# Performance work log

Hardware: AMD Instinct MI355X
Metric: run time of the kernel (lower is better)

Reference implementation:

```python
import jax, jax.numpy as jnp
import numpy as np

TEMP = 1.0
NUM_HEADS = 4


def tropical_linear(x, W, b, temperature=TEMP):
    # x: (..., in), W: (out, in), b: (out,)
    # y_i = T * logsumexp_j((W_ij + x_j)/T) + b_i  (soft tropical max-plus)
    z = W + x[..., None, :]                      # (..., out, in) broadcast tensor
    y = temperature * jax.nn.logsumexp(z / temperature, axis=-1)
    return y + b


def setup_inputs() -> dict:
    key = jax.random.key(0)
    ks = jax.random.split(key, 5)
    B, S, E = 32, 64, 256  # seq_len == head_dim (= E / num_heads) required by original code
    x = jax.random.normal(ks[0], (B, S, E), dtype=jnp.float32)
    mk = lambda k: 0.1 * jax.random.normal(k, (E, E), dtype=jnp.float32)
    zb = jnp.zeros((E,), dtype=jnp.float32)
    return {
        "x": x,
        "Wq": mk(ks[1]), "bq": zb,
        "Wk": mk(ks[2]), "bk": zb,
        "Wv": mk(ks[3]), "bv": zb,
        "Wo": mk(ks[4]), "bo": zb,
    }


def reference(x, Wq, bq, Wk, bk, Wv, bv, Wo, bo):
    B, S, E = x.shape
    H = NUM_HEADS
    D = E // H  # == S by construction (required by original matmul)

    q = tropical_linear(x, Wq, bq)  # (B,S,E)
    k = tropical_linear(x, Wk, bk)
    v = tropical_linear(x, Wv, bv)

    # (B,S,E) -> (B,H,S,D)
    split = lambda t: t.reshape(B, S, H, D).transpose(0, 2, 1, 3)
    q, k, v = split(q), split(k), split(v)

    # Original: (q.unsqueeze(-1) + k.unsqueeze(-2).transpose(-1,-2)).sum(-1)
    # Both operands are (B,H,S,D,1) -> scores == q + k elementwise, shape (B,H,S,D).
    scores = q + k
    attn = jax.nn.softmax(scores / TEMP, axis=-1)  # (B,H,S,D)

    # matmul (B,H,S,D) @ (B,H,S,D) valid since D == S
    out = jnp.einsum('bhsd,bhde->bhse', attn, v)   # (B,H,S,D)
    out = out.transpose(0, 2, 1, 3).reshape(B, S, E)
    return tropical_linear(out, Wo, bo)
```

## Files before the change

kernel.cpp:

```cpp
#include <hip/hip_runtime.h>

constexpr int ED = 256;
constexpr int SD = 64;
constexpr int BD = 32;
constexpr int NROWS = BD * SD;

typedef _Float16 half8 __attribute__((ext_vector_type(8)));
typedef float floatx4 __attribute__((ext_vector_type(4)));

__device__ inline unsigned short f2h(float f) {
  union { _Float16 h; unsigned short u; } c;
  c.h = (_Float16)f;
  return c.u;
}

__global__ __launch_bounds__(256) void expT_swz_kernel(
    const float* __restrict__ Wq, const float* __restrict__ Wk,
    const float* __restrict__ Wv, const float* __restrict__ Wo,
    unsigned short* __restrict__ EqS, unsigned short* __restrict__ EkS,
    unsigned short* __restrict__ EvS, unsigned short* __restrict__ EoS)
{
  int z = blockIdx.y;
  const float* W = (z == 0) ? Wq : (z == 1) ? Wk : (z == 2) ? Wv : Wo;
  unsigned short* out = (z == 0) ? EqS : (z == 1) ? EkS : (z == 2) ? EvS : EoS;
  int t = threadIdx.x;
  int n = blockIdx.x * 8 + (t >> 5), kl = t & 31;
#pragma unroll
  for (int kk = 0; kk < 8; ++kk)
    out[(kk * 256 + n) * 32 + kl] = f2h(__expf(W[n * ED + 32 * kk + kl]));
}

__global__ __launch_bounds__(256, 2) void qkv_mfma_kernel(
    const float* __restrict__ x,
    const unsigned short* __restrict__ EqS, const unsigned short* __restrict__ EkS,
    const unsigned short* __restrict__ EvS,
    const float* __restrict__ bq, const float* __restrict__ bk,
    const float* __restrict__ bv,
    unsigned short* __restrict__ AS, unsigned short* __restrict__ VS)
{
  int t = threadIdx.x;
  int w = t >> 6, lane = t & 63;
  int mt = blockIdx.x >> 2, h = blockIdx.x & 3;
  int row0 = mt * 16;

  __shared__ unsigned short aswz[8 * 512];
  __shared__ float fbuf[3][16][65];
  __shared__ float Mrow[16];

  float4 xv[4];
#pragma unroll
  for (int i = 0; i < 4; ++i)
    xv[i] = *(const float4*)&x[(size_t)(row0 + 4 * w + i) * ED + lane * 4];

  int bb = ((h * 64 + w * 16 + (lane & 15)) << 2) + (lane >> 4);
  const half8* BQ = (const half8*)EqS;
  const half8* BK = (const half8*)EkS;
  const half8* BV = (const half8*)EvS;
  half8 bqf[8], bkf[8], bvf[8];
#pragma unroll
  for (int kk = 0; kk < 8; ++kk) {
    bqf[kk] = BQ[kk * 1024 + bb];
    bkf[kk] = BK[kk * 1024 + bb];
    bvf[kk] = BV[kk * 1024 + bb];
  }

#pragma unroll
  for (int i = 0; i < 4; ++i) {
    int r = 4 * w + i;
    float m = fmaxf(fmaxf(xv[i].x, xv[i].y), fmaxf(xv[i].z, xv[i].w));
#pragma unroll
    for (int off = 32; off > 0; off >>= 1) m = fmaxf(m, __shfl_xor(m, off));
    ushort4 pk;
    pk.x = f2h(__expf(xv[i].x - m));
    pk.y = f2h(__expf(xv[i].y - m));
    pk.z = f2h(__expf(xv[i].z - m));
    pk.w = f2h(__expf(xv[i].w - m));
    int k0 = lane * 4;
    int idx = (k0 >> 5) * 512 + ((k0 >> 3) & 3) * 128 + r * 8 + (k0 & 7);
    *(ushort4*)&aswz[idx] = pk;
    if (lane == 0) Mrow[r] = m;
  }
  __syncthreads();

  half8 afrag[8];
#pragma unroll
  for (int kk = 0; kk < 8; ++kk)
    afrag[kk] = *(const half8*)&aswz[kk * 512 + lane * 8];

  floatx4 accq = {0.f, 0.f, 0.f, 0.f};
  floatx4 acck = {0.f, 0.f, 0.f, 0.f};
  floatx4 accv = {0.f, 0.f, 0.f, 0.f};
#pragma unroll
  for (int kk = 0; kk < 8; ++kk) {
    accq = __builtin_amdgcn_mfma_f32_16x16x32_f16(afrag[kk], bqf[kk], accq, 0, 0, 0);
    acck = __builtin_amdgcn_mfma_f32_16x16x32_f16(afrag[kk], bkf[kk], acck, 0, 0, 0);
    accv = __builtin_amdgcn_mfma_f32_16x16x32_f16(afrag[kk], bvf[kk], accv, 0, 0, 0);
  }

  {
    int c = w * 16 + (lane & 15);
    int rb = (lane >> 4) * 4;
#pragma unroll
    for (int reg = 0; reg < 4; ++reg) {
      fbuf[0][rb + reg][c] = accq[reg];
      fbuf[1][rb + reg][c] = acck[reg];
      fbuf[2][rb + reg][c] = accv[reg];
    }
  }
  __syncthreads();

  int cg = h * 64 + lane;
  float bqv = bq[cg], bkv = bk[cg], bvv = bv[cg];
  int b = row0 >> 6;
  int mt16 = (row0 >> 4) & 3;
  size_t asBase = (size_t)(((b * 4 + mt16) * 4) + h) * 1024
                + (lane >> 5) * 512 + ((lane >> 3) & 3) * 128 + (lane & 7);
#pragma unroll
  for (int i = 0; i < 4; ++i) {
    int r = 4 * w + i;
    float Mr = Mrow[r];
    float qv = Mr + __logf(fbuf[0][r][lane]) + bqv;
    float kv = Mr + __logf(fbuf[1][r][lane]) + bkv;
    float vv = Mr + __logf(fbuf[2][r][lane]) + bvv;
    int d = mt16 * 16 + r;
    VS[(size_t)(b * 2 + (d >> 5)) * 8192 + cg * 32 + ((d >> 3) & 3) * 8 + (d & 7)]
        = f2h(vv);
    float s = qv + kv;
    float sm = s;
#pragma unroll
    for (int off = 32; off > 0; off >>= 1) sm = fmaxf(sm, __shfl_xor(sm, off));
    float ex = __expf(s - sm);
    float den = ex;
#pragma unroll
    for (int off = 32; off > 0; off >>= 1) den += __shfl_xor(den, off);
    AS[asBase + r * 8] = f2h(ex / den);
  }
}

__global__ __launch_bounds__(256, 2) void avo_mfma_kernel(
    const unsigned short* __restrict__ AS, const unsigned short* __restrict__ VS,
    const unsigned short* __restrict__ EoS, const float* __restrict__ bo,
    float* __restrict__ y)
{
  int t = threadIdx.x, w = t >> 6, lane = t & 63;
  int blk = blockIdx.x;
  int b = blk >> 3, mt = (blk >> 1) & 3, hf = blk & 1;
  int row0 = b * 64 + mt * 16;
  int q = lane >> 4, nl = lane & 15;

  __shared__ float obuf[16][260];
  __shared__ unsigned short easwz[8 * 512];
  __shared__ float Mrow[16];

  const half8* AS8 = (const half8*)(AS + (size_t)(((b * 4 + mt) * 4) + w) * 1024);
  const half8* VS8 = (const half8*)VS;
  half8 af0 = AS8[lane], af1 = AS8[64 + lane];
  floatx4 acc[4];
#pragma unroll
  for (int nt = 0; nt < 4; ++nt) acc[nt] = (floatx4){0.f, 0.f, 0.f, 0.f};
#pragma unroll
  for (int nt = 0; nt < 4; ++nt) {
    int n = w * 64 + nt * 16 + nl;
    half8 b0 = VS8[(size_t)(b * 2 + 0) * 1024 + n * 4 + q];
    half8 b1 = VS8[(size_t)(b * 2 + 1) * 1024 + n * 4 + q];
    acc[nt] = __builtin_amdgcn_mfma_f32_16x16x32_f16(af0, b0, acc[nt], 0, 0, 0);
    acc[nt] = __builtin_amdgcn_mfma_f32_16x16x32_f16(af1, b1, acc[nt], 0, 0, 0);
  }
  int rb = q * 4;
#pragma unroll
  for (int nt = 0; nt < 4; ++nt)
#pragma unroll
    for (int reg = 0; reg < 4; ++reg)
      obuf[rb + reg][w * 64 + nt * 16 + nl] = acc[nt][reg];
  __syncthreads();

#pragma unroll
  for (int i = 0; i < 4; ++i) {
    int r = 4 * w + i;
    float4 o4 = *(const float4*)&obuf[r][lane * 4];
    float m = fmaxf(fmaxf(o4.x, o4.y), fmaxf(o4.z, o4.w));
#pragma unroll
    for (int off = 32; off > 0; off >>= 1) m = fmaxf(m, __shfl_xor(m, off));
    ushort4 pk;
    pk.x = f2h(__expf(o4.x - m));
    pk.y = f2h(__expf(o4.y - m));
    pk.z = f2h(__expf(o4.z - m));
    pk.w = f2h(__expf(o4.w - m));
    int k0 = lane * 4;
    int idx = (k0 >> 5) * 512 + ((k0 >> 3) & 3) * 128 + r * 8 + (k0 & 7);
    *(ushort4*)&easwz[idx] = pk;
    if (lane == 0) Mrow[r] = m;
  }
  __syncthreads();

  half8 af2[8];
#pragma unroll
  for (int kk = 0; kk < 8; ++kk)
    af2[kk] = *(const half8*)&easwz[kk * 512 + lane * 8];
  const half8* BO = (const half8*)EoS;
  floatx4 acc2[2];
  acc2[0] = (floatx4){0.f, 0.f, 0.f, 0.f};
  acc2[1] = (floatx4){0.f, 0.f, 0.f, 0.f};
#pragma unroll
  for (int kk = 0; kk < 8; ++kk) {
#pragma unroll
    for (int nt = 0; nt < 2; ++nt) {
      int n = hf * 128 + w * 32 + nt * 16 + nl;
      acc2[nt] = __builtin_amdgcn_mfma_f32_16x16x32_f16(
          af2[kk], BO[kk * 1024 + n * 4 + q], acc2[nt], 0, 0, 0);
    }
  }
#pragma unroll
  for (int nt = 0; nt < 2; ++nt)
#pragma unroll
    for (int reg = 0; reg < 4; ++reg)
      obuf[rb + reg][hf * 128 + w * 32 + nt * 16 + nl] = acc2[nt][reg];
  __syncthreads();

  int c0 = hf * 128 + lane * 2;
  float2 bo2 = *(const float2*)&bo[c0];
#pragma unroll
  for (int i = 0; i < 4; ++i) {
    int r = 4 * w + i;
    float2 f2 = *(const float2*)&obuf[r][c0];
    float M = Mrow[r];
    float2 y2;
    y2.x = M + __logf(f2.x) + bo2.x;
    y2.y = M + __logf(f2.y) + bo2.y;
    *(float2*)&y[(size_t)(row0 + r) * ED + c0] = y2;
  }
}

extern "C" void kernel_launch(void* const* d_in, const int* in_sizes, int n_in,
                              void* d_out, int out_size, void* d_ws, size_t ws_size,
                              hipStream_t stream) {
  const float* x  = (const float*)d_in[0];
  const float* Wq = (const float*)d_in[1];
  const float* bq = (const float*)d_in[2];
  const float* Wk = (const float*)d_in[3];
  const float* bk = (const float*)d_in[4];
  const float* Wv = (const float*)d_in[5];
  const float* bv = (const float*)d_in[6];
  const float* Wo = (const float*)d_in[7];
  const float* bo = (const float*)d_in[8];
  float* y = (float*)d_out;

  char* ws = (char*)d_ws;
  unsigned short* EqS = (unsigned short*)(ws);
  unsigned short* EkS = (unsigned short*)(ws + 131072);
  unsigned short* EvS = (unsigned short*)(ws + 262144);
  unsigned short* EoS = (unsigned short*)(ws + 393216);
  unsigned short* AS  = (unsigned short*)(ws + 524288);
  unsigned short* VS  = (unsigned short*)(ws + 524288 + 1048576);

  expT_swz_kernel<<<dim3(32, 4), 256, 0, stream>>>(Wq, Wk, Wv, Wo,
                                                   EqS, EkS, EvS, EoS);
  qkv_mfma_kernel<<<512, 256, 0, stream>>>(x, EqS, EkS, EvS, bq, bk, bv,
                                           AS, VS);
  avo_mfma_kernel<<<256, 256, 0, stream>>>(AS, VS, EoS, bo, y);
}
```

Measured before the change: 86.20 us.

## Fuse QKV projection, attention and output projection into one per-batch kernel

Replaces the two MFMA kernels with a single kernel that handles one batch element per 512-thread block. Q/K/V, the softmax, attn·V and the output tropical projection all stay in shared memory, so the global round trip for the A and V intermediates and one launch are gone. The cost is a grid of only 32 blocks on a many-CU GPU, which leaves most compute units idle. Each wave also now streams all of the 128 output columns' weights through registers, raising register pressure.

```diff
diff --git a/kernel.cpp b/kernel.cpp
--- a/kernel.cpp
+++ b/kernel.cpp
@@ -1,9 +1,6 @@
 #include <hip/hip_runtime.h>
 
 constexpr int ED = 256;
-constexpr int SD = 64;
-constexpr int BD = 32;
-constexpr int NROWS = BD * SD;
 
 typedef _Float16 half8 __attribute__((ext_vector_type(8)));
 typedef float floatx4 __attribute__((ext_vector_type(4)));
@@ -30,43 +27,33 @@
     out[(kk * 256 + n) * 32 + kl] = f2h(__expf(W[n * ED + 32 * kk + kl]));
 }
 
-__global__ __launch_bounds__(256, 2) void qkv_mfma_kernel(
+__global__ __launch_bounds__(512, 1) void fused_attn_kernel(
     const float* __restrict__ x,
     const unsigned short* __restrict__ EqS, const unsigned short* __restrict__ EkS,
-    const unsigned short* __restrict__ EvS,
+    const unsigned short* __restrict__ EvS, const unsigned short* __restrict__ EoS,
     const float* __restrict__ bq, const float* __restrict__ bk,
-    const float* __restrict__ bv,
-    unsigned short* __restrict__ AS, unsigned short* __restrict__ VS)
+    const float* __restrict__ bv, const float* __restrict__ bo,
+    float* __restrict__ y)
 {
-  int t = threadIdx.x;
-  int w = t >> 6, lane = t & 63;
-  int mt = blockIdx.x >> 2, h = blockIdx.x & 3;
-  int row0 = mt * 16;
-
-  __shared__ unsigned short aswz[8 * 512];
-  __shared__ float fbuf[3][16][65];
-  __shared__ float Mrow[16];
-
-  float4 xv[4];
-#pragma unroll
-  for (int i = 0; i < 4; ++i)
-    xv[i] = *(const float4*)&x[(size_t)(row0 + 4 * w + i) * ED + lane * 4];
-
-  int bb = ((h * 64 + w * 16 + (lane & 15)) << 2) + (lane >> 4);
-  const half8* BQ = (const half8*)EqS;
-  const half8* BK = (const half8*)EkS;
-  const half8* BV = (const half8*)EvS;
-  half8 bqf[8], bkf[8], bvf[8];
-#pragma unroll
-  for (int kk = 0; kk < 8; ++kk) {
-    bqf[kk] = BQ[kk * 1024 + bb];
-    bkf[kk] = BK[kk * 1024 + bb];
-    bvf[kk] = BV[kk * 1024 + bb];
-  }
-
-#pragma unroll
-  for (int i = 0; i < 4; ++i) {
-    int r = 4 * w + i;
+  int t = threadIdx.x, w = t >> 6, lane = t & 63;
+  int b = blockIdx.x;
+  int q = lane >> 4, nl = lane & 15;
+  int rb = q * 4;
+
+  __shared__ unsigned short xoswz[4][4096];
+  __shared__ unsigned short aswz[4][4096];
+  __shared__ unsigned short vswz[4][4096];
+  __shared__ float Mrow[64];
+  __shared__ float pmax[8][64];
+  __shared__ float Omax[64];
+
+  float4 xv[8];
+#pragma unroll
+  for (int i = 0; i < 8; ++i)
+    xv[i] = *(const float4*)&x[(size_t)(b * 64 + w * 8 + i) * ED + lane * 4];
+#pragma unroll
+  for (int i = 0; i < 8; ++i) {
+    int r = w * 8 + i;
     float m = fmaxf(fmaxf(xv[i].x, xv[i].y), fmaxf(xv[i].z, xv[i].w));
 #pragma unroll
     for (int off = 32; off > 0; off >>= 1) m = fmaxf(m, __shfl_xor(m, off));
@@ -76,158 +63,180 @@
     pk.z = f2h(__expf(xv[i].z - m));
     pk.w = f2h(__expf(xv[i].w - m));
     int k0 = lane * 4;
-    int idx = (k0 >> 5) * 512 + ((k0 >> 3) & 3) * 128 + r * 8 + (k0 & 7);
-    *(ushort4*)&aswz[idx] = pk;
+    int idx = (k0 >> 5) * 512 + ((k0 >> 3) & 3) * 128 + (r & 15) * 8 + (k0 & 7);
+    *(ushort4*)&xoswz[r >> 4][idx] = pk;
     if (lane == 0) Mrow[r] = m;
   }
   __syncthreads();
 
-  half8 afrag[8];
-#pragma unroll
-  for (int kk = 0; kk < 8; ++kk)
-    afrag[kk] = *(const half8*)&aswz[kk * 512 + lane * 8];
-
-  floatx4 accq = {0.f, 0.f, 0.f, 0.f};
-  floatx4 acck = {0.f, 0.f, 0.f, 0.f};
-  floatx4 accv = {0.f, 0.f, 0.f, 0.f};
-#pragma unroll
-  for (int kk = 0; kk < 8; ++kk) {
-    accq = __builtin_amdgcn_mfma_f32_16x16x32_f16(afrag[kk], bqf[kk], accq, 0, 0, 0);
-    acck = __builtin_amdgcn_mfma_f32_16x16x32_f16(afrag[kk], bkf[kk], acck, 0, 0, 0);
-    accv = __builtin_amdgcn_mfma_f32_16x16x32_f16(afrag[kk], bvf[kk], accv, 0, 0, 0);
-  }
-
-  {
-    int c = w * 16 + (lane & 15);
-    int rb = (lane >> 4) * 4;
-#pragma unroll
-    for (int reg = 0; reg < 4; ++reg) {
-      fbuf[0][rb + reg][c] = accq[reg];
-      fbuf[1][rb + reg][c] = acck[reg];
-      fbuf[2][rb + reg][c] = accv[reg];
-    }
-  }
-  __syncthreads();
-
-  int cg = h * 64 + lane;
-  float bqv = bq[cg], bkv = bk[cg], bvv = bv[cg];
-  int b = row0 >> 6;
-  int mt16 = (row0 >> 4) & 3;
-  size_t asBase = (size_t)(((b * 4 + mt16) * 4) + h) * 1024
-                + (lane >> 5) * 512 + ((lane >> 3) & 3) * 128 + (lane & 7);
-#pragma unroll
-  for (int i = 0; i < 4; ++i) {
-    int r = 4 * w + i;
-    float Mr = Mrow[r];
-    float qv = Mr + __logf(fbuf[0][r][lane]) + bqv;
-    float kv = Mr + __logf(fbuf[1][r][lane]) + bkv;
-    float vv = Mr + __logf(fbuf[2][r][lane]) + bvv;
-    int d = mt16 * 16 + r;
-    VS[(size_t)(b * 2 + (d >> 5)) * 8192 + cg * 32 + ((d >> 3) & 3) * 8 + (d & 7)]
-        = f2h(vv);
-    float s = qv + kv;
-    float sm = s;
-#pragma unroll
-    for (int off = 32; off > 0; off >>= 1) sm = fmaxf(sm, __shfl_xor(sm, off));
-    float ex = __expf(s - sm);
-    float den = ex;
-#pragma unroll
-    for (int off = 32; off > 0; off >>= 1) den += __shfl_xor(den, off);
-    AS[asBase + r * 8] = f2h(ex / den);
-  }
-}
-
-__global__ __launch_bounds__(256, 2) void avo_mfma_kernel(
-    const unsigned short* __restrict__ AS, const unsigned short* __restrict__ VS,
-    const unsigned short* __restrict__ EoS, const float* __restrict__ bo,
-    float* __restrict__ y)
-{
-  int t = threadIdx.x, w = t >> 6, lane = t & 63;
-  int blk = blockIdx.x;
-  int b = blk >> 3, mt = (blk >> 1) & 3, hf = blk & 1;
-  int row0 = b * 64 + mt * 16;
-  int q = lane >> 4, nl = lane & 15;
-
-  __shared__ float obuf[16][260];
-  __shared__ unsigned short easwz[8 * 512];
-  __shared__ float Mrow[16];
-
-  const half8* AS8 = (const half8*)(AS + (size_t)(((b * 4 + mt) * 4) + w) * 1024);
-  const half8* VS8 = (const half8*)VS;
-  half8 af0 = AS8[lane], af1 = AS8[64 + lane];
-  floatx4 acc[4];
-#pragma unroll
-  for (int nt = 0; nt < 4; ++nt) acc[nt] = (floatx4){0.f, 0.f, 0.f, 0.f};
-#pragma unroll
-  for (int nt = 0; nt < 4; ++nt) {
-    int n = w * 64 + nt * 16 + nl;
-    half8 b0 = VS8[(size_t)(b * 2 + 0) * 1024 + n * 4 + q];
-    half8 b1 = VS8[(size_t)(b * 2 + 1) * 1024 + n * 4 + q];
-    acc[nt] = __builtin_amdgcn_mfma_f32_16x16x32_f16(af0, b0, acc[nt], 0, 0, 0);
-    acc[nt] = __builtin_amdgcn_mfma_f32_16x16x32_f16(af1, b1, acc[nt], 0, 0, 0);
-  }
-  int rb = q * 4;
-#pragma unroll
-  for (int nt = 0; nt < 4; ++nt)
-#pragma unroll
-    for (int reg = 0; reg < 4; ++reg)
-      obuf[rb + reg][w * 64 + nt * 16 + nl] = acc[nt][reg];
-  __syncthreads();
-
-#pragma unroll
-  for (int i = 0; i < 4; ++i) {
-    int r = 4 * w + i;
-    float4 o4 = *(const float4*)&obuf[r][lane * 4];
-    float m = fmaxf(fmaxf(o4.x, o4.y), fmaxf(o4.z, o4.w));
-#pragma unroll
-    for (int off = 32; off > 0; off >>= 1) m = fmaxf(m, __shfl_xor(m, off));
-    ushort4 pk;
-    pk.x = f2h(__expf(o4.x - m));
-    pk.y = f2h(__expf(o4.y - m));
-    pk.z = f2h(__expf(o4.z - m));
-    pk.w = f2h(__expf(o4.w - m));
-    int k0 = lane * 4;
-    int idx = (k0 >> 5) * 512 + ((k0 >> 3) & 3) * 128 + r * 8 + (k0 & 7);
-    *(ushort4*)&easwz[idx] = pk;
-    if (lane == 0) Mrow[r] = m;
-  }
-  __syncthreads();
-
+  int mt = w >> 1, hf = w & 1;
+  const half8* XA = (const half8*)xoswz[mt];
+  half8 af[8];
+#pragma unroll
+  for (int kk = 0; kk < 8; ++kk) af[kk] = XA[kk * 64 + lane];
+
+  float Mr[4];
+#pragma unroll
+  for (int reg = 0; reg < 4; ++reg) Mr[reg] = Mrow[mt * 16 + rb + reg];
+
+  float bqv[8], bkv[8], bvv[8];
+#pragma unroll
+  for (int nt = 0; nt < 8; ++nt) {
+    int c = hf * 128 + nt * 16 + nl;
+    bqv[nt] = bq[c]; bkv[nt] = bk[c]; bvv[nt] = bv[c];
+  }
+
+  const half8* BQ = (const half8*)EqS;
+  const half8* BK = (const half8*)EkS;
+  const half8* BV = (const half8*)EvS;
+  floatx4 aq[8], ak[8], av[8];
+#pragma unroll
+  for (int nt = 0; nt < 8; ++nt) {
+    aq[nt] = (floatx4){0.f, 0.f, 0.f, 0.f};
+    ak[nt] = (floatx4){0.f, 0.f, 0.f, 0.f};
+    av[nt] = (floatx4){0.f, 0.f, 0.f, 0.f};
+  }
+#pragma unroll
+  for (int nt = 0; nt < 8; ++nt) {
+    int n4 = (hf * 128 + nt * 16 + nl) * 4 + q;
+#pragma unroll
+    for (int kk = 0; kk < 8; ++kk) {
+      aq[nt] = __builtin_amdgcn_mfma_f32_16x16x32_f16(af[kk], BQ[kk * 1024 + n4], aq[nt], 0, 0, 0);
+      ak[nt] = __builtin_amdgcn_mfma_f32_16x16x32_f16(af[kk], BK[kk * 1024 + n4], ak[nt], 0, 0, 0);
+      av[nt] = __builtin_amdgcn_mfma_f32_16x16x32_f16(af[kk], BV[kk * 1024 + n4], av[nt], 0, 0, 0);
+    }
+  }
+
+#pragma unroll
+  for (int nt = 0; nt < 8; ++nt) {
+    int c = hf * 128 + nt * 16 + nl;
+    int hd = c >> 6, n = c & 63;
+#pragma unroll
+    for (int reg = 0; reg < 4; ++reg) {
+      int r = mt * 16 + rb + reg;
+      float vv = Mr[reg] + __logf(av[nt][reg]) + bvv[nt];
+      vswz[hd][((r >> 5) * 64 + n) * 32 + ((r >> 3) & 3) * 8 + (r & 7)] = f2h(vv);
+    }
+  }
+#pragma unroll
+  for (int hh = 0; hh < 2; ++hh) {
+    int hd = hf * 2 + hh;
+#pragma unroll
+    for (int reg = 0; reg < 4; ++reg) {
+      float s[4];
+#pragma unroll
+      for (int j = 0; j < 4; ++j) {
+        int nt = hh * 4 + j;
+        s[j] = __logf(aq[nt][reg]) + __logf(ak[nt][reg]) + bqv[nt] + bkv[nt];
+      }
+      float mm = fmaxf(fmaxf(s[0], s[1]), fmaxf(s[2], s[3]));
+#pragma unroll
+      for (int off = 8; off > 0; off >>= 1) mm = fmaxf(mm, __shfl_xor(mm, off));
+      float ex[4], den = 0.f;
+#pragma unroll
+      for (int j = 0; j < 4; ++j) { ex[j] = __expf(s[j] - mm); den += ex[j]; }
+#pragma unroll
+      for (int off = 8; off > 0; off >>= 1) den += __shfl_xor(den, off);
+      float rden = 1.0f / den;
+#pragma unroll
+      for (int j = 0; j < 4; ++j) {
+        int d = j * 16 + nl;
+        aswz[hd][mt * 1024 + (d >> 5) * 512 + ((d >> 3) & 3) * 128
+                 + (rb + reg) * 8 + (d & 7)] = f2h(ex[j] * rden);
+      }
+    }
+  }
+  __syncthreads();
+
+  int hd = w >> 1, nh = w & 1;
+  const half8* AH = (const half8*)aswz[hd];
+  half8 afa[4][2];
+#pragma unroll
+  for (int m2 = 0; m2 < 4; ++m2)
+#pragma unroll
+    for (int kk = 0; kk < 2; ++kk)
+      afa[m2][kk] = AH[m2 * 128 + kk * 64 + lane];
+  const half8* VH = (const half8*)vswz[hd];
+  half8 bfv[2][2];
+#pragma unroll
+  for (int nt = 0; nt < 2; ++nt) {
+    int n = nh * 32 + nt * 16 + nl;
+#pragma unroll
+    for (int kk = 0; kk < 2; ++kk) bfv[nt][kk] = VH[(kk * 64 + n) * 4 + q];
+  }
+  floatx4 oacc[4][2];
+#pragma unroll
+  for (int m2 = 0; m2 < 4; ++m2)
+#pragma unroll
+    for (int nt = 0; nt < 2; ++nt) oacc[m2][nt] = (floatx4){0.f, 0.f, 0.f, 0.f};
+#pragma unroll
+  for (int m2 = 0; m2 < 4; ++m2)
+#pragma unroll
+    for (int nt = 0; nt < 2; ++nt) {
+      oacc[m2][nt] = __builtin_amdgcn_mfma_f32_16x16x32_f16(afa[m2][0], bfv[nt][0], oacc[m2][nt], 0, 0, 0);
+      oacc[m2][nt] = __builtin_amdgcn_mfma_f32_16x16x32_f16(afa[m2][1], bfv[nt][1], oacc[m2][nt], 0, 0, 0);
+    }
+
+#pragma unroll
+  for (int m2 = 0; m2 < 4; ++m2)
+#pragma unroll
+    for (int reg = 0; reg < 4; ++reg) {
+      float pm = fmaxf(oacc[m2][0][reg], oacc[m2][1][reg]);
+#pragma unroll
+      for (int off = 8; off > 0; off >>= 1) pm = fmaxf(pm, __shfl_xor(pm, off));
+      if (nl == 0) pmax[w][m2 * 16 + rb + reg] = pm;
+    }
+  __syncthreads();
+  if (t < 64) {
+    float m = pmax[0][t];
+#pragma unroll
+    for (int j = 1; j < 8; ++j) m = fmaxf(m, pmax[j][t]);
+    Omax[t] = m;
+  }
+  __syncthreads();
+
+#pragma unroll
+  for (int m2 = 0; m2 < 4; ++m2)
+#pragma unroll
+    for (int nt = 0; nt < 2; ++nt) {
+      int c = hd * 64 + nh * 32 + nt * 16 + nl;
+#pragma unroll
+      for (int reg = 0; reg < 4; ++reg) {
+        float e = __expf(oacc[m2][nt][reg] - Omax[m2 * 16 + rb + reg]);
+        xoswz[m2][(c >> 5) * 512 + ((c >> 3) & 3) * 128 + (rb + reg) * 8 + (c & 7)]
+            = f2h(e);
+      }
+    }
+  __syncthreads();
+
+  const half8* OA = (const half8*)xoswz[mt];
   half8 af2[8];
 #pragma unroll
-  for (int kk = 0; kk < 8; ++kk)
-    af2[kk] = *(const half8*)&easwz[kk * 512 + lane * 8];
+  for (int kk = 0; kk < 8; ++kk) af2[kk] = OA[kk * 64 + lane];
   const half8* BO = (const half8*)EoS;
-  floatx4 acc2[2];
-  acc2[0] = (floatx4){0.f, 0.f, 0.f, 0.f};
-  acc2[1] = (floatx4){0.f, 0.f, 0.f, 0.f};
-#pragma unroll
-  for (int kk = 0; kk < 8; ++kk) {
-#pragma unroll
-    for (int nt = 0; nt < 2; ++nt) {
-      int n = hf * 128 + w * 32 + nt * 16 + nl;
-      acc2[nt] = __builtin_amdgcn_mfma_f32_16x16x32_f16(
-          af2[kk], BO[kk * 1024 + n * 4 + q], acc2[nt], 0, 0, 0);
-    }
-  }
-#pragma unroll
-  for (int nt = 0; nt < 2; ++nt)
-#pragma unroll
-    for (int reg = 0; reg < 4; ++reg)
-      obuf[rb + reg][hf * 128 + w * 32 + nt * 16 + nl] = acc2[nt][reg];
-  __syncthreads();
-
-  int c0 = hf * 128 + lane * 2;
-  float2 bo2 = *(const float2*)&bo[c0];
-#pragma unroll
-  for (int i = 0; i < 4; ++i) {
-    int r = 4 * w + i;
-    float2 f2 = *(const float2*)&obuf[r][c0];
-    float M = Mrow[r];
-    float2 y2;
-    y2.x = M + __logf(f2.x) + bo2.x;
-    y2.y = M + __logf(f2.y) + bo2.y;
-    *(float2*)&y[(size_t)(row0 + r) * ED + c0] = y2;
+  floatx4 acc2[8];
+#pragma unroll
+  for (int nt = 0; nt < 8; ++nt) acc2[nt] = (floatx4){0.f, 0.f, 0.f, 0.f};
+#pragma unroll
+  for (int nt = 0; nt < 8; ++nt) {
+    int n4 = (hf * 128 + nt * 16 + nl) * 4 + q;
+#pragma unroll
+    for (int kk = 0; kk < 8; ++kk)
+      acc2[nt] = __builtin_amdgcn_mfma_f32_16x16x32_f16(af2[kk], BO[kk * 1024 + n4], acc2[nt], 0, 0, 0);
+  }
+
+  float MrO[4];
+#pragma unroll
+  for (int reg = 0; reg < 4; ++reg) MrO[reg] = Omax[mt * 16 + rb + reg];
+#pragma unroll
+  for (int nt = 0; nt < 8; ++nt) {
+    int c = hf * 128 + nt * 16 + nl;
+    float bov = bo[c];
+#pragma unroll
+    for (int reg = 0; reg < 4; ++reg) {
+      int r = mt * 16 + rb + reg;
+      y[(size_t)(b * 64 + r) * ED + c] = MrO[reg] + __logf(acc2[nt][reg]) + bov;
+    }
   }
 }
 
@@ -250,12 +259,9 @@
   unsigned short* EkS = (unsigned short*)(ws + 131072);
   unsigned short* EvS = (unsigned short*)(ws + 262144);
   unsigned short* EoS = (unsigned short*)(ws + 393216);
-  unsigned short* AS  = (unsigned short*)(ws + 524288);
-  unsigned short* VS  = (unsigned short*)(ws + 524288 + 1048576);
 
   expT_swz_kernel<<<dim3(32, 4), 256, 0, stream>>>(Wq, Wk, Wv, Wo,
                                                    EqS, EkS, EvS, EoS);
-  qkv_mfma_kernel<<<512, 256, 0, stream>>>(x, EqS, EkS, EvS, bq, bk, bv,
-                                           AS, VS);
-  avo_mfma_kernel<<<256, 256, 0, stream>>>(AS, VS, EoS, bo, y);
-}
+  fused_attn_kernel<<<32, 512, 0, stream>>>(x, EqS, EkS, EvS, EoS,
+                                            bq, bk, bv, bo, y);
+}
```

Result: slower. 113.5 us (+31.7%).

## Fuse weight exponentiation into QKV and output MFMA kernels, drop precompute launch

Applied to the files above, without the earlier changes.

Removes the separate kernel that exponentiated and swizzled the weights into fp16 workspace buffers. The QKV and output kernels now load the fp32 weights directly and compute exp into MFMA B fragments in registers. This saves one kernel launch and its workspace round trip. In exchange, each block redundantly reads fp32 weights (twice the bytes of fp16) and recomputes the exponentials, and the per-thread strided loads are less coalesced.

```diff
diff --git a/kernel.cpp b/kernel.cpp
--- a/kernel.cpp
+++ b/kernel.cpp
@@ -1,9 +1,6 @@
 #include <hip/hip_runtime.h>
 
 constexpr int ED = 256;
-constexpr int SD = 64;
-constexpr int BD = 32;
-constexpr int NROWS = BD * SD;
 
 typedef _Float16 half8 __attribute__((ext_vector_type(8)));
 typedef float floatx4 __attribute__((ext_vector_type(4)));
@@ -14,26 +11,21 @@
   return c.u;
 }
 
-__global__ __launch_bounds__(256) void expT_swz_kernel(
-    const float* __restrict__ Wq, const float* __restrict__ Wk,
-    const float* __restrict__ Wv, const float* __restrict__ Wo,
-    unsigned short* __restrict__ EqS, unsigned short* __restrict__ EkS,
-    unsigned short* __restrict__ EvS, unsigned short* __restrict__ EoS)
-{
-  int z = blockIdx.y;
-  const float* W = (z == 0) ? Wq : (z == 1) ? Wk : (z == 2) ? Wv : Wo;
-  unsigned short* out = (z == 0) ? EqS : (z == 1) ? EkS : (z == 2) ? EvS : EoS;
-  int t = threadIdx.x;
-  int n = blockIdx.x * 8 + (t >> 5), kl = t & 31;
-#pragma unroll
-  for (int kk = 0; kk < 8; ++kk)
-    out[(kk * 256 + n) * 32 + kl] = f2h(__expf(W[n * ED + 32 * kk + kl]));
+__device__ inline half8 expfrag(const float* __restrict__ p) {
+  float4 a = *(const float4*)p;
+  float4 b = *(const float4*)(p + 4);
+  half8 r;
+  r[0] = (_Float16)__expf(a.x); r[1] = (_Float16)__expf(a.y);
+  r[2] = (_Float16)__expf(a.z); r[3] = (_Float16)__expf(a.w);
+  r[4] = (_Float16)__expf(b.x); r[5] = (_Float16)__expf(b.y);
+  r[6] = (_Float16)__expf(b.z); r[7] = (_Float16)__expf(b.w);
+  return r;
 }
 
 __global__ __launch_bounds__(256, 2) void qkv_mfma_kernel(
     const float* __restrict__ x,
-    const unsigned short* __restrict__ EqS, const unsigned short* __restrict__ EkS,
-    const unsigned short* __restrict__ EvS,
+    const float* __restrict__ Wq, const float* __restrict__ Wk,
+    const float* __restrict__ Wv,
     const float* __restrict__ bq, const float* __restrict__ bk,
     const float* __restrict__ bv,
     unsigned short* __restrict__ AS, unsigned short* __restrict__ VS)
@@ -52,16 +44,17 @@
   for (int i = 0; i < 4; ++i)
     xv[i] = *(const float4*)&x[(size_t)(row0 + 4 * w + i) * ED + lane * 4];
 
-  int bb = ((h * 64 + w * 16 + (lane & 15)) << 2) + (lane >> 4);
-  const half8* BQ = (const half8*)EqS;
-  const half8* BK = (const half8*)EkS;
-  const half8* BV = (const half8*)EvS;
+  int ncol = h * 64 + w * 16 + (lane & 15);
+  int q8 = (lane >> 4) * 8;
+  const float* pWq = Wq + (size_t)ncol * ED + q8;
+  const float* pWk = Wk + (size_t)ncol * ED + q8;
+  const float* pWv = Wv + (size_t)ncol * ED + q8;
   half8 bqf[8], bkf[8], bvf[8];
 #pragma unroll
   for (int kk = 0; kk < 8; ++kk) {
-    bqf[kk] = BQ[kk * 1024 + bb];
-    bkf[kk] = BK[kk * 1024 + bb];
-    bvf[kk] = BV[kk * 1024 + bb];
+    bqf[kk] = expfrag(pWq + 32 * kk);
+    bkf[kk] = expfrag(pWk + 32 * kk);
+    bvf[kk] = expfrag(pWv + 32 * kk);
   }
 
 #pragma unroll
@@ -139,7 +132,7 @@
 
 __global__ __launch_bounds__(256, 2) void avo_mfma_kernel(
     const unsigned short* __restrict__ AS, const unsigned short* __restrict__ VS,
-    const unsigned short* __restrict__ EoS, const float* __restrict__ bo,
+    const float* __restrict__ Wo, const float* __restrict__ bo,
     float* __restrict__ y)
 {
   int t = threadIdx.x, w = t >> 6, lane = t & 63;
@@ -151,6 +144,15 @@
   __shared__ float obuf[16][260];
   __shared__ unsigned short easwz[8 * 512];
   __shared__ float Mrow[16];
+
+  int q8 = q * 8;
+  const float* pWo = Wo + (size_t)(hf * 128 + w * 32 + nl) * ED + q8;
+  half8 bof[8][2];
+#pragma unroll
+  for (int nt = 0; nt < 2; ++nt)
+#pragma unroll
+    for (int kk = 0; kk < 8; ++kk)
+      bof[kk][nt] = expfrag(pWo + (size_t)nt * 16 * ED + 32 * kk);
 
   const half8* AS8 = (const half8*)(AS + (size_t)(((b * 4 + mt) * 4) + w) * 1024);
   const half8* VS8 = (const half8*)VS;
@@ -197,18 +199,15 @@
 #pragma unroll
   for (int kk = 0; kk < 8; ++kk)
     af2[kk] = *(const half8*)&easwz[kk * 512 + lane * 8];
-  const half8* BO = (const half8*)EoS;
   floatx4 acc2[2];
   acc2[0] = (floatx4){0.f, 0.f, 0.f, 0.f};
   acc2[1] = (floatx4){0.f, 0.f, 0.f, 0.f};
 #pragma unroll
   for (int kk = 0; kk < 8; ++kk) {
 #pragma unroll
-    for (int nt = 0; nt < 2; ++nt) {
-      int n = hf * 128 + w * 32 + nt * 16 + nl;
+    for (int nt = 0; nt < 2; ++nt)
       acc2[nt] = __builtin_amdgcn_mfma_f32_16x16x32_f16(
-          af2[kk], BO[kk * 1024 + n * 4 + q], acc2[nt], 0, 0, 0);
-    }
+          af2[kk], bof[kk][nt], acc2[nt], 0, 0, 0);
   }
 #pragma unroll
   for (int nt = 0; nt < 2; ++nt)
@@ -246,16 +245,9 @@
   float* y = (float*)d_out;
 
   char* ws = (char*)d_ws;
-  unsigned short* EqS = (unsigned short*)(ws);
-  unsigned short* EkS = (unsigned short*)(ws + 131072);
-  unsigned short* EvS = (unsigned short*)(ws + 262144);
-  unsigned short* EoS = (unsigned short*)(ws + 393216);
-  unsigned short* AS  = (unsigned short*)(ws + 524288);
-  unsigned short* VS  = (unsigned short*)(ws + 524288 + 1048576);
-
-  expT_swz_kernel<<<dim3(32, 4), 256, 0, stream>>>(Wq, Wk, Wv, Wo,
-                                                   EqS, EkS, EvS, EoS);
-  qkv_mfma_kernel<<<512, 256, 0, stream>>>(x, EqS, EkS, EvS, bq, bk, bv,
-                                           AS, VS);
-  avo_mfma_kernel<<<256, 256, 0, stream>>>(AS, VS, EoS, bo, y);
-}
+  unsigned short* AS = (unsigned short*)(ws);
+  unsigned short* VS = (unsigned short*)(ws + 1048576);
+
+  qkv_mfma_kernel<<<512, 256, 0, stream>>>(x, Wq, Wk, Wv, bq, bk, bv, AS, VS);
+  avo_mfma_kernel<<<256, 256, 0, stream>>>(AS, VS, Wo, bo, y);
+}
```

After: 95.95 us. +11.3%, slower.

## Fuse three kernels into one cooperative persistent kernel with grid syncs

Applied to the files above, without the earlier changes.

Merges the weight-exponentiation, QKV projection and attention/output-projection kernels into a single cooperative launch of 512 blocks. Two grid-wide barriers stand in for the kernel boundaries, and shared memory is reused through a union. The output stage is repartitioned so each block handles a quarter of the columns, matching the 512-block grid. This removes two launch gaps and lets the x exponentiation overlap with the weight exp stage, but adds grid.sync costs and depends on all 512 blocks being co-resident.

```diff
diff --git a/kernel.cpp b/kernel.cpp
--- a/kernel.cpp
+++ b/kernel.cpp
@@ -1,9 +1,9 @@
 #include <hip/hip_runtime.h>
+#include <hip/hip_cooperative_groups.h>
+
+namespace cg = cooperative_groups;
 
 constexpr int ED = 256;
-constexpr int SD = 64;
-constexpr int BD = 32;
-constexpr int NROWS = BD * SD;
 
 typedef _Float16 half8 __attribute__((ext_vector_type(8)));
 typedef float floatx4 __attribute__((ext_vector_type(4)));
@@ -14,54 +14,50 @@
   return c.u;
 }
 
-__global__ __launch_bounds__(256) void expT_swz_kernel(
+struct P1sm {
+  unsigned short aswz[8 * 512];
+  float fbuf[3][16][65];
+  float Mrow[16];
+};
+struct P2sm {
+  float obuf[16][260];
+  unsigned short easwz[8 * 512];
+  float Mrow[16];
+};
+
+__global__ __launch_bounds__(256, 2) void tropical_fused(
+    const float* __restrict__ x,
     const float* __restrict__ Wq, const float* __restrict__ Wk,
     const float* __restrict__ Wv, const float* __restrict__ Wo,
-    unsigned short* __restrict__ EqS, unsigned short* __restrict__ EkS,
-    unsigned short* __restrict__ EvS, unsigned short* __restrict__ EoS)
+    const float* __restrict__ bq, const float* __restrict__ bk,
+    const float* __restrict__ bv, const float* __restrict__ bo,
+    unsigned short* __restrict__ ES, unsigned short* __restrict__ AS,
+    unsigned short* __restrict__ VS, float* __restrict__ y)
 {
-  int z = blockIdx.y;
-  const float* W = (z == 0) ? Wq : (z == 1) ? Wk : (z == 2) ? Wv : Wo;
-  unsigned short* out = (z == 0) ? EqS : (z == 1) ? EkS : (z == 2) ? EvS : EoS;
-  int t = threadIdx.x;
-  int n = blockIdx.x * 8 + (t >> 5), kl = t & 31;
-#pragma unroll
-  for (int kk = 0; kk < 8; ++kk)
-    out[(kk * 256 + n) * 32 + kl] = f2h(__expf(W[n * ED + 32 * kk + kl]));
-}
-
-__global__ __launch_bounds__(256, 2) void qkv_mfma_kernel(
-    const float* __restrict__ x,
-    const unsigned short* __restrict__ EqS, const unsigned short* __restrict__ EkS,
-    const unsigned short* __restrict__ EvS,
-    const float* __restrict__ bq, const float* __restrict__ bk,
-    const float* __restrict__ bv,
-    unsigned short* __restrict__ AS, unsigned short* __restrict__ VS)
-{
-  int t = threadIdx.x;
-  int w = t >> 6, lane = t & 63;
-  int mt = blockIdx.x >> 2, h = blockIdx.x & 3;
+  __shared__ union { P1sm p1; P2sm p2; } sm;
+  int t = threadIdx.x, w = t >> 6, lane = t & 63;
+  int bid = blockIdx.x;
+  cg::grid_group grid = cg::this_grid();
+
+  int mt = bid >> 2, h = bid & 3;
   int row0 = mt * 16;
-
-  __shared__ unsigned short aswz[8 * 512];
-  __shared__ float fbuf[3][16][65];
-  __shared__ float Mrow[16];
 
   float4 xv[4];
 #pragma unroll
   for (int i = 0; i < 4; ++i)
     xv[i] = *(const float4*)&x[(size_t)(row0 + 4 * w + i) * ED + lane * 4];
 
-  int bb = ((h * 64 + w * 16 + (lane & 15)) << 2) + (lane >> 4);
-  const half8* BQ = (const half8*)EqS;
-  const half8* BK = (const half8*)EkS;
-  const half8* BV = (const half8*)EvS;
-  half8 bqf[8], bkf[8], bvf[8];
-#pragma unroll
-  for (int kk = 0; kk < 8; ++kk) {
-    bqf[kk] = BQ[kk * 1024 + bb];
-    bkf[kk] = BK[kk * 1024 + bb];
-    bvf[kk] = BV[kk * 1024 + bb];
+  {
+    int z = bid >> 7;
+    const float* Wz = (z == 0) ? Wq : (z == 1) ? Wk : (z == 2) ? Wv : Wo;
+    unsigned short* outz = ES + z * 65536;
+    int n = (bid & 127) * 2 + (t >> 7);
+    int kl = t & 31;
+#pragma unroll
+    for (int i = 0; i < 2; ++i) {
+      int kk = ((t >> 5) & 3) + 4 * i;
+      outz[(kk * 256 + n) * 32 + kl] = f2h(__expf(Wz[n * ED + 32 * kk + kl]));
+    }
   }
 
 #pragma unroll
@@ -77,157 +73,151 @@
     pk.w = f2h(__expf(xv[i].w - m));
     int k0 = lane * 4;
     int idx = (k0 >> 5) * 512 + ((k0 >> 3) & 3) * 128 + r * 8 + (k0 & 7);
-    *(ushort4*)&aswz[idx] = pk;
-    if (lane == 0) Mrow[r] = m;
-  }
-  __syncthreads();
-
-  half8 afrag[8];
-#pragma unroll
-  for (int kk = 0; kk < 8; ++kk)
-    afrag[kk] = *(const half8*)&aswz[kk * 512 + lane * 8];
-
-  floatx4 accq = {0.f, 0.f, 0.f, 0.f};
-  floatx4 acck = {0.f, 0.f, 0.f, 0.f};
-  floatx4 accv = {0.f, 0.f, 0.f, 0.f};
-#pragma unroll
-  for (int kk = 0; kk < 8; ++kk) {
-    accq = __builtin_amdgcn_mfma_f32_16x16x32_f16(afrag[kk], bqf[kk], accq, 0, 0, 0);
-    acck = __builtin_amdgcn_mfma_f32_16x16x32_f16(afrag[kk], bkf[kk], acck, 0, 0, 0);
-    accv = __builtin_amdgcn_mfma_f32_16x16x32_f16(afrag[kk], bvf[kk], accv, 0, 0, 0);
-  }
+    *(ushort4*)&sm.p1.aswz[idx] = pk;
+    if (lane == 0) sm.p1.Mrow[r] = m;
+  }
+
+  grid.sync();
 
   {
-    int c = w * 16 + (lane & 15);
-    int rb = (lane >> 4) * 4;
-#pragma unroll
-    for (int reg = 0; reg < 4; ++reg) {
-      fbuf[0][rb + reg][c] = accq[reg];
-      fbuf[1][rb + reg][c] = acck[reg];
-      fbuf[2][rb + reg][c] = accv[reg];
-    }
-  }
-  __syncthreads();
-
-  int cg = h * 64 + lane;
-  float bqv = bq[cg], bkv = bk[cg], bvv = bv[cg];
-  int b = row0 >> 6;
-  int mt16 = (row0 >> 4) & 3;
-  size_t asBase = (size_t)(((b * 4 + mt16) * 4) + h) * 1024
-                + (lane >> 5) * 512 + ((lane >> 3) & 3) * 128 + (lane & 7);
-#pragma unroll
-  for (int i = 0; i < 4; ++i) {
-    int r = 4 * w + i;
-    float Mr = Mrow[r];
-    float qv = Mr + __logf(fbuf[0][r][lane]) + bqv;
-    float kv = Mr + __logf(fbuf[1][r][lane]) + bkv;
-    float vv = Mr + __logf(fbuf[2][r][lane]) + bvv;
-    int d = mt16 * 16 + r;
-    VS[(size_t)(b * 2 + (d >> 5)) * 8192 + cg * 32 + ((d >> 3) & 3) * 8 + (d & 7)]
-        = f2h(vv);
-    float s = qv + kv;
-    float sm = s;
-#pragma unroll
-    for (int off = 32; off > 0; off >>= 1) sm = fmaxf(sm, __shfl_xor(sm, off));
-    float ex = __expf(s - sm);
-    float den = ex;
-#pragma unroll
-    for (int off = 32; off > 0; off >>= 1) den += __shfl_xor(den, off);
-    AS[asBase + r * 8] = f2h(ex / den);
-  }
-}
-
-__global__ __launch_bounds__(256, 2) void avo_mfma_kernel(
-    const unsigned short* __restrict__ AS, const unsigned short* __restrict__ VS,
-    const unsigned short* __restrict__ EoS, const float* __restrict__ bo,
-    float* __restrict__ y)
-{
-  int t = threadIdx.x, w = t >> 6, lane = t & 63;
-  int blk = blockIdx.x;
-  int b = blk >> 3, mt = (blk >> 1) & 3, hf = blk & 1;
-  int row0 = b * 64 + mt * 16;
-  int q = lane >> 4, nl = lane & 15;
-
-  __shared__ float obuf[16][260];
-  __shared__ unsigned short easwz[8 * 512];
-  __shared__ float Mrow[16];
-
-  const half8* AS8 = (const half8*)(AS + (size_t)(((b * 4 + mt) * 4) + w) * 1024);
-  const half8* VS8 = (const half8*)VS;
-  half8 af0 = AS8[lane], af1 = AS8[64 + lane];
-  floatx4 acc[4];
-#pragma unroll
-  for (int nt = 0; nt < 4; ++nt) acc[nt] = (floatx4){0.f, 0.f, 0.f, 0.f};
-#pragma unroll
-  for (int nt = 0; nt < 4; ++nt) {
-    int n = w * 64 + nt * 16 + nl;
-    half8 b0 = VS8[(size_t)(b * 2 + 0) * 1024 + n * 4 + q];
-    half8 b1 = VS8[(size_t)(b * 2 + 1) * 1024 + n * 4 + q];
-    acc[nt] = __builtin_amdgcn_mfma_f32_16x16x32_f16(af0, b0, acc[nt], 0, 0, 0);
-    acc[nt] = __builtin_amdgcn_mfma_f32_16x16x32_f16(af1, b1, acc[nt], 0, 0, 0);
-  }
-  int rb = q * 4;
-#pragma unroll
-  for (int nt = 0; nt < 4; ++nt)
+    int bb = ((h * 64 + w * 16 + (lane & 15)) << 2) + (lane >> 4);
+    const half8* BQ = (const half8*)ES;
+    const half8* BK = (const half8*)(ES + 65536);
+    const half8* BV = (const half8*)(ES + 131072);
+    half8 bqf[8], bkf[8], bvf[8];
+#pragma unroll
+    for (int kk = 0; kk < 8; ++kk) {
+      bqf[kk] = BQ[kk * 1024 + bb];
+      bkf[kk] = BK[kk * 1024 + bb];
+      bvf[kk] = BV[kk * 1024 + bb];
+    }
+
+    half8 afrag[8];
+#pragma unroll
+    for (int kk = 0; kk < 8; ++kk)
+      afrag[kk] = *(const half8*)&sm.p1.aswz[kk * 512 + lane * 8];
+
+    floatx4 accq = {0.f, 0.f, 0.f, 0.f};
+    floatx4 acck = {0.f, 0.f, 0.f, 0.f};
+    floatx4 accv = {0.f, 0.f, 0.f, 0.f};
+#pragma unroll
+    for (int kk = 0; kk < 8; ++kk) {
+      accq = __builtin_amdgcn_mfma_f32_16x16x32_f16(afrag[kk], bqf[kk], accq, 0, 0, 0);
+      acck = __builtin_amdgcn_mfma_f32_16x16x32_f16(afrag[kk], bkf[kk], acck, 0, 0, 0);
+      accv = __builtin_amdgcn_mfma_f32_16x16x32_f16(afrag[kk], bvf[kk], accv, 0, 0, 0);
+    }
+
+    {
+      int c = w * 16 + (lane & 15);
+      int rb = (lane >> 4) * 4;
+#pragma unroll
+      for (int reg = 0; reg < 4; ++reg) {
+        sm.p1.fbuf[0][rb + reg][c] = accq[reg];
+        sm.p1.fbuf[1][rb + reg][c] = acck[reg];
+        sm.p1.fbuf[2][rb + reg][c] = accv[reg];
+      }
+    }
+    __syncthreads();
+
+    int cg_ = h * 64 + lane;
+    float bqv = bq[cg_], bkv = bk[cg_], bvv = bv[cg_];
+    int b = row0 >> 6;
+    int mt16 = (row0 >> 4) & 3;
+    size_t asBase = (size_t)(((b * 4 + mt16) * 4) + h) * 1024
+                  + (lane >> 5) * 512 + ((lane >> 3) & 3) * 128 + (lane & 7);
+#pragma unroll
+    for (int i = 0; i < 4; ++i) {
+      int r = 4 * w + i;
+      float Mr = sm.p1.Mrow[r];
+      float qv = Mr + __logf(sm.p1.fbuf[0][r][lane]) + bqv;
+      float kv = Mr + __logf(sm.p1.fbuf[1][r][lane]) + bkv;
+      float vv = Mr + __logf(sm.p1.fbuf[2][r][lane]) + bvv;
+      int d = mt16 * 16 + r;
+      VS[(size_t)(b * 2 + (d >> 5)) * 8192 + cg_ * 32 + ((d >> 3) & 3) * 8 + (d & 7)]
+          = f2h(vv);
+      float s = qv + kv;
+      float smx = s;
+#pragma unroll
+      for (int off = 32; off > 0; off >>= 1) smx = fmaxf(smx, __shfl_xor(smx, off));
+      float ex = __expf(s - smx);
+      float den = ex;
+#pragma unroll
+      for (int off = 32; off > 0; off >>= 1) den += __shfl_xor(den, off);
+      AS[asBase + r * 8] = f2h(ex / den);
+    }
+  }
+
+  grid.sync();
+
+  {
+    int b2 = bid >> 4, mt2 = (bid >> 2) & 3, qtr = bid & 3;
+    int row2 = b2 * 64 + mt2 * 16;
+    int q = lane >> 4, nl = lane & 15;
+    int rb = q * 4;
+
+    const half8* AS8 = (const half8*)(AS + (size_t)(((b2 * 4 + mt2) * 4) + w) * 1024);
+    const half8* VS8 = (const half8*)VS;
+    half8 af0 = AS8[lane], af1 = AS8[64 + lane];
+    floatx4 acc[4];
+#pragma unroll
+    for (int nt = 0; nt < 4; ++nt) acc[nt] = (floatx4){0.f, 0.f, 0.f, 0.f};
+#pragma unroll
+    for (int nt = 0; nt < 4; ++nt) {
+      int n = w * 64 + nt * 16 + nl;
+      half8 b0 = VS8[(size_t)(b2 * 2 + 0) * 1024 + n * 4 + q];
+      half8 b1 = VS8[(size_t)(b2 * 2 + 1) * 1024 + n * 4 + q];
+      acc[nt] = __builtin_amdgcn_mfma_f32_16x16x32_f16(af0, b0, acc[nt], 0, 0, 0);
+      acc[nt] = __builtin_amdgcn_mfma_f32_16x16x32_f16(af1, b1, acc[nt], 0, 0, 0);
+    }
+#pragma unroll
+    for (int nt = 0; nt < 4; ++nt)
+#pragma unroll
+      for (int reg = 0; reg < 4; ++reg)
+        sm.p2.obuf[rb + reg][w * 64 + nt * 16 + nl] = acc[nt][reg];
+    __syncthreads();
+
+#pragma unroll
+    for (int i = 0; i < 4; ++i) {
+      int r = 4 * w + i;
+      float4 o4 = *(const float4*)&sm.p2.obuf[r][lane * 4];
+      float m = fmaxf(fmaxf(o4.x, o4.y), fmaxf(o4.z, o4.w));
+#pragma unroll
+      for (int off = 32; off > 0; off >>= 1) m = fmaxf(m, __shfl_xor(m, off));
+      ushort4 pk;
+      pk.x = f2h(__expf(o4.x - m));
+      pk.y = f2h(__expf(o4.y - m));
+      pk.z = f2h(__expf(o4.z - m));
+      pk.w = f2h(__expf(o4.w - m));
+      int k0 = lane * 4;
+      int idx = (k0 >> 5) * 512 + ((k0 >> 3) & 3) * 128 + r * 8 + (k0 & 7);
+      *(ushort4*)&sm.p2.easwz[idx] = pk;
+      if (lane == 0) sm.p2.Mrow[r] = m;
+    }
+    __syncthreads();
+
+    half8 af2[8];
+#pragma unroll
+    for (int kk = 0; kk < 8; ++kk)
+      af2[kk] = *(const half8*)&sm.p2.easwz[kk * 512 + lane * 8];
+    const half8* BO = (const half8*)(ES + 3 * 65536);
+    int n = qtr * 64 + w * 16 + nl;
+    floatx4 acc2 = {0.f, 0.f, 0.f, 0.f};
+#pragma unroll
+    for (int kk = 0; kk < 8; ++kk)
+      acc2 = __builtin_amdgcn_mfma_f32_16x16x32_f16(
+          af2[kk], BO[kk * 1024 + n * 4 + q], acc2, 0, 0, 0);
 #pragma unroll
     for (int reg = 0; reg < 4; ++reg)
-      obuf[rb + reg][w * 64 + nt * 16 + nl] = acc[nt][reg];
-  __syncthreads();
-
-#pragma unroll
-  for (int i = 0; i < 4; ++i) {
-    int r = 4 * w + i;
-    float4 o4 = *(const float4*)&obuf[r][lane * 4];
-    float m = fmaxf(fmaxf(o4.x, o4.y), fmaxf(o4.z, o4.w));
-#pragma unroll
-    for (int off = 32; off > 0; off >>= 1) m = fmaxf(m, __shfl_xor(m, off));
-    ushort4 pk;
-    pk.x = f2h(__expf(o4.x - m));
-    pk.y = f2h(__expf(o4.y - m));
-    pk.z = f2h(__expf(o4.z - m));
-    pk.w = f2h(__expf(o4.w - m));
-    int k0 = lane * 4;
-    int idx = (k0 >> 5) * 512 + ((k0 >> 3) & 3) * 128 + r * 8 + (k0 & 7);
-    *(ushort4*)&easwz[idx] = pk;
-    if (lane == 0) Mrow[r] = m;
-  }
-  __syncthreads();
-
-  half8 af2[8];
-#pragma unroll
-  for (int kk = 0; kk < 8; ++kk)
-    af2[kk] = *(const half8*)&easwz[kk * 512 + lane * 8];
-  const half8* BO = (const half8*)EoS;
-  floatx4 acc2[2];
-  acc2[0] = (floatx4){0.f, 0.f, 0.f, 0.f};
-  acc2[1] = (floatx4){0.f, 0.f, 0.f, 0.f};
-#pragma unroll
-  for (int kk = 0; kk < 8; ++kk) {
-#pragma unroll
-    for (int nt = 0; nt < 2; ++nt) {
-      int n = hf * 128 + w * 32 + nt * 16 + nl;
-      acc2[nt] = __builtin_amdgcn_mfma_f32_16x16x32_f16(
-          af2[kk], BO[kk * 1024 + n * 4 + q], acc2[nt], 0, 0, 0);
-    }
-  }
-#pragma unroll
-  for (int nt = 0; nt < 2; ++nt)
-#pragma unroll
-    for (int reg = 0; reg < 4; ++reg)
-      obuf[rb + reg][hf * 128 + w * 32 + nt * 16 + nl] = acc2[nt][reg];
-  __syncthreads();
-
-  int c0 = hf * 128 + lane * 2;
-  float2 bo2 = *(const float2*)&bo[c0];
-#pragma unroll
-  for (int i = 0; i < 4; ++i) {
-    int r = 4 * w + i;
-    float2 f2 = *(const float2*)&obuf[r][c0];
-    float M = Mrow[r];
-    float2 y2;
-    y2.x = M + __logf(f2.x) + bo2.x;
-    y2.y = M + __logf(f2.y) + bo2.y;
-    *(float2*)&y[(size_t)(row0 + r) * ED + c0] = y2;
+      sm.p2.obuf[rb + reg][n] = acc2[reg];
+    __syncthreads();
+
+    int c = qtr * 64 + lane;
+    float bov = bo[c];
+#pragma unroll
+    for (int i = 0; i < 4; ++i) {
+      int r = 4 * w + i;
+      y[(size_t)(row2 + r) * ED + c] = sm.p2.Mrow[r] + __logf(sm.p2.obuf[r][c]) + bov;
+    }
   }
 }
 
@@ -246,16 +236,13 @@
   float* y = (float*)d_out;
 
   char* ws = (char*)d_ws;
-  unsigned short* EqS = (unsigned short*)(ws);
-  unsigned short* EkS = (unsigned short*)(ws + 131072);
-  unsigned short* EvS = (unsigned short*)(ws + 262144);
-  unsigned short* EoS = (unsigned short*)(ws + 393216);
-  unsigned short* AS  = (unsigned short*)(ws + 524288);
-  unsigned short* VS  = (unsigned short*)(ws + 524288 + 1048576);
-
-  expT_swz_kernel<<<dim3(32, 4), 256, 0, stream>>>(Wq, Wk, Wv, Wo,
-                                                   EqS, EkS, EvS, EoS);
-  qkv_mfma_kernel<<<512, 256, 0, stream>>>(x, EqS, EkS, EvS, bq, bk, bv,
-                                           AS, VS);
-  avo_mfma_kernel<<<256, 256, 0, stream>>>(AS, VS, EoS, bo, y);
+  unsigned short* ES = (unsigned short*)(ws);
+  unsigned short* AS = (unsigned short*)(ws + 524288);
+  unsigned short* VS = (unsigned short*)(ws + 524288 + 1048576);
+
+  void* args[] = {(void*)&x, (void*)&Wq, (void*)&Wk, (void*)&Wv, (void*)&Wo,
+                  (void*)&bq, (void*)&bk, (void*)&bv, (void*)&bo,
+                  (void*)&ES, (void*)&AS, (void*)&VS, (void*)&y};
+  hipLaunchCooperativeKernel((void*)tropical_fused, dim3(512), dim3(256),
+                             args, 0, stream);
 }
```

Result: slower. 205.9 us (+138.8%).
